# Performance work log

Hardware: AMD Instinct MI355X
Metric: run time of the kernel (lower is better)

Reference implementation:

```python
import jax, jax.numpy as jnp
import numpy as np

B, T, C, L = 512, 512, 96, 64   # batch, time steps, num classes (incl. blank), max label len
BLANK = C - 1                   # keras ctc_batch_cost uses last class as blank
EPS = 1e-7                      # epsilon added before log, as in ctc_batch_cost
NEG = -1e30                     # log-space -inf surrogate


def setup_inputs():
    key = jax.random.key(0)
    k1, k2, k3 = jax.random.split(key, 3)
    # y_pred is a softmax output: positive, rows sum to 1
    u = jax.random.uniform(k1, (B, T, C), dtype=jnp.float32, minval=0.1, maxval=1.0)
    y_pred = u / jnp.sum(u, axis=-1, keepdims=True)
    # labels in [0, BLANK), variable lengths, padded with -1 (as the layer expects)
    labels = jax.random.randint(k2, (B, L), 0, C - 1, dtype=jnp.int32)
    lens = jax.random.randint(k3, (B,), L // 2, L + 1, dtype=jnp.int32)
    y_true = jnp.where(jnp.arange(L)[None, :] < lens[:, None], labels, -1)
    return {"y_true": y_true, "y_pred": y_pred}


def _ctc_loss(y_true, y_pred):
    """Per-example CTC negative log-likelihood (forward DP in log space)."""
    y_true = y_true.astype(jnp.int32)
    lbl_len = jnp.sum((y_true != -1).astype(jnp.int32), axis=-1)          # (B,)
    labels = jnp.where(y_true != -1, y_true, 0)                            # (B,L)

    S = 2 * L + 1
    # extended label: blank, l0, blank, l1, ..., blank
    ext = jnp.full((B, S), BLANK, dtype=jnp.int32).at[:, 1::2].set(labels)  # (B,S)
    ext_m2 = jnp.pad(ext[:, :-2], ((0, 0), (2, 0)), constant_values=BLANK)
    can_skip = (ext != BLANK) & (ext != ext_m2)                             # (B,S)

    lp = jnp.log(y_pred.astype(jnp.float32) + EPS)   # (B,T,C) log-probs
    lp_t = jnp.swapaxes(lp, 0, 1)                    # (T,B,C) for scan over time

    emit0 = jnp.take_along_axis(lp_t[0], ext, axis=1)                       # (B,S)
    alpha0 = (jnp.full((B, S), NEG, dtype=jnp.float32)
              .at[:, 0].set(emit0[:, 0])
              .at[:, 1].set(emit0[:, 1]))

    def step(alpha, lpt):
        a1 = jnp.pad(alpha[:, :-1], ((0, 0), (1, 0)), constant_values=NEG)
        a2 = jnp.pad(alpha[:, :-2], ((0, 0), (2, 0)), constant_values=NEG)
        a2 = jnp.where(can_skip, a2, NEG)
        m = jnp.maximum(alpha, jnp.maximum(a1, a2))
        lse = m + jnp.log(jnp.exp(alpha - m) + jnp.exp(a1 - m) + jnp.exp(a2 - m))
        alpha_new = lse + jnp.take_along_axis(lpt, ext, axis=1)
        return alpha_new, None

    alphaT, _ = jax.lax.scan(step, alpha0, lp_t[1:])

    # total log-prob ends at last blank (s=2*len) or last label (s=2*len-1)
    i_blank = (2 * lbl_len)[:, None]
    i_label = jnp.maximum(2 * lbl_len - 1, 0)[:, None]
    a_b = jnp.take_along_axis(alphaT, i_blank, axis=1)[:, 0]
    a_l = jnp.take_along_axis(alphaT, i_label, axis=1)[:, 0]
    return -jnp.logaddexp(a_b, a_l)                                         # (B,)


def reference(y_true, y_pred):
    # layer adds tf.reduce_mean(ctc_batch_cost(...)) as the model loss
    return jnp.mean(_ctc_loss(y_true, y_pred))
```

## Files before the change

### kernel.cpp

```cpp
#include <hip/hip_runtime.h>


#define B_ 512
#define T_ 512
#define C_ 96
#define L_ 64
#define BLANK_ 95
#define EPSF 1e-7f
#define LN2F 0.69314718055994530942f

#define BARRIER() asm volatile("s_waitcnt lgkmcnt(0)\n\ts_barrier" ::: "memory")

template <int CTRL>
__device__ __forceinline__ float dpp_mov(float x) {
    return __int_as_float(
        __builtin_amdgcn_update_dpp(0, __float_as_int(x), CTRL, 0xF, 0xF, true));
}

__device__ __forceinline__ float wave_max(float m) {
    m = fmaxf(m, dpp_mov<0x111>(m));
    m = fmaxf(m, dpp_mov<0x112>(m));
    m = fmaxf(m, dpp_mov<0x114>(m));
    m = fmaxf(m, dpp_mov<0x118>(m));
    m = fmaxf(m, dpp_mov<0x142>(m));
    m = fmaxf(m, dpp_mov<0x143>(m));
    return __int_as_float(__builtin_amdgcn_readlane(__float_as_int(m), 63));
}

__launch_bounds__(256, 1)
__global__ void ctc_loss_kernel(const int* __restrict__ y_true,
                                const float* __restrict__ y_pred,
                                float* __restrict__ out) {
    const int b = blockIdx.x;
    const int tid = threadIdx.x;
    const int wid = tid >> 6;
    const int lane = tid & 63;

    constexpr int U = 8;
    constexpr int NCH = T_ / U;
    constexpr int CHW = U * C_;

    __shared__ __align__(16) float smem[2 * CHW];

    const float* __restrict__ gb = y_pred + (size_t)b * T_ * C_ + lane * 4;

    int len = 0, lab = 0;
    bool cs = false;
    float a_even = 0.0f, a_odd = 0.0f, a128 = 0.0f;
    int accum = -96;
    float4 rg[3];

    if (wid == 0) {
        const int yv = y_true[b * L_ + lane];
        const unsigned long long act = __ballot(yv != -1);
        len = __popcll(act);
        lab = (yv == -1) ? 0 : yv;
        const int lab_prev = __shfl_up(lab, 1);
        cs = (lane == 0) ? true : (lab != lab_prev);
        a_even = (lane == 0) ? 0x1.0p96f : 0.0f;
    } else {
        const int p = wid - 1;
        const int c0 = (p == 0) ? 0 : p;
#pragma unroll
        for (int j = 0; j < 3; ++j)
            rg[j] = *reinterpret_cast<const float4*>(gb + c0 * CHW + j * 256);
        if (p == 0) {
#pragma unroll
            for (int j = 0; j < 3; ++j)
                *reinterpret_cast<float4*>(&smem[(j * 64 + lane) * 4]) = rg[j];
#pragma unroll
            for (int j = 0; j < 3; ++j)
                rg[j] = *reinterpret_cast<const float4*>(gb + 3 * CHW + j * 256);
        }
    }

    for (int i = 0; i < NCH; ++i) {
        BARRIER();
        if (wid == 0) {
            const float* sl = smem + (i & 1) * CHW;
            float pl[U], pb[U], mpl[U];
#pragma unroll
            for (int k = 0; k < U; ++k) {
                pl[k] = sl[k * C_ + lab] + EPSF;
                pb[k] = sl[k * C_ + BLANK_] + EPSF;
                mpl[k] = cs ? pl[k] : 0.0f;
            }
#pragma unroll
            for (int k = 0; k < U; ++k) {
                const float po = dpp_mov<0x138>(a_odd);
                const float ne = fmaf(po, pb[k], a_even * pb[k]);
                const float no = fmaf(po, mpl[k], (a_odd + a_even) * pl[k]);
                a128 = fmaf(a_odd, pb[k], a128 * pb[k]);
                a_even = ne;
                a_odd = no;
            }
            const float mv = wave_max(fmaxf(fmaxf(a_even, a_odd), a128));
            const int e = ((__float_as_int(mv) >> 23) & 0xFF) - 126;
            const int kk = 96 - e;
            a_even = ldexpf(a_even, kk);
            a_odd = ldexpf(a_odd, kk);
            a128 = ldexpf(a128, kk);
            accum -= kk;
        } else {
            const int p = wid - 1;
            const int cw = i + 1;
            if (cw < NCH && (cw % 3) == p) {
                float* dst = smem + (cw & 1) * CHW;
#pragma unroll
                for (int j = 0; j < 3; ++j)
                    *reinterpret_cast<float4*>(&dst[(j * 64 + lane) * 4]) = rg[j];
                const int nc = cw + 3;
                if (nc < NCH) {
#pragma unroll
                    for (int j = 0; j < 3; ++j)
                        rg[j] = *reinterpret_cast<const float4*>(
                            gb + nc * CHW + j * 256);
                }
            }
        }
    }

    if (wid == 0) {
        const float al = __shfl(a_odd, len - 1);
        const float ab = (len < L_) ? __shfl(a_even, len)
                                    : __shfl(a128, 63);
        if (lane == 0) {
            const float loss = -LN2F * (log2f(ab + al) + (float)accum);
            atomicAdd(out, loss * (1.0f / B_));
        }
    }
}

extern "C" void kernel_launch(void* const* d_in, const int* in_sizes, int n_in,
                              void* d_out, int out_size, void* d_ws, size_t ws_size,
                              hipStream_t stream) {
    const int* y_true = (const int*)d_in[0];
    const float* y_pred = (const float*)d_in[1];
    float* out = (float*)d_out;
    hipMemsetAsync(out, 0, sizeof(float), stream);
    ctc_loss_kernel<<<B_, 256, 0, stream>>>(y_true, y_pred, out);
}
```

Before: 182.8 us.

## Software-pipeline LDS probability reads into registers with a four-slot shared ring

The single consumer wave now loads the next chunk's label and blank probabilities from shared memory into a second register set while it computes the current chunk. This takes LDS read latency off the serial recurrence. To allow it, the shared buffer grows from two to four chunk slots and the producer waves fill two chunks ahead. The block is split into separate consumer and producer loops, each hitting the same number of barriers. This costs more shared memory and more consumer registers, and the last iteration does one extra unused LDS read.

Measured after the change: 176.6 us. 1.04x faster.

```diff
diff --git a/kernel.cpp b/kernel.cpp
--- a/kernel.cpp
+++ b/kernel.cpp
@@ -10,6 +10,7 @@
 #define LN2F 0.69314718055994530942f
 
 #define BARRIER() asm volatile("s_waitcnt lgkmcnt(0)\n\ts_barrier" ::: "memory")
+#define SCHED_FENCE() asm volatile("" ::: "memory")
 
 template <int CTRL>
 __device__ __forceinline__ float dpp_mov(float x) {
@@ -40,93 +41,121 @@
     constexpr int NCH = T_ / U;
     constexpr int CHW = U * C_;
 
-    __shared__ __align__(16) float smem[2 * CHW];
+    __shared__ __align__(16) float smem[4 * CHW];
 
     const float* __restrict__ gb = y_pred + (size_t)b * T_ * C_ + lane * 4;
-
-    int len = 0, lab = 0;
-    bool cs = false;
-    float a_even = 0.0f, a_odd = 0.0f, a128 = 0.0f;
-    int accum = -96;
-    float4 rg[3];
 
     if (wid == 0) {
         const int yv = y_true[b * L_ + lane];
         const unsigned long long act = __ballot(yv != -1);
-        len = __popcll(act);
-        lab = (yv == -1) ? 0 : yv;
+        const int len = __popcll(act);
+        const int lab = (yv == -1) ? 0 : yv;
         const int lab_prev = __shfl_up(lab, 1);
-        cs = (lane == 0) ? true : (lab != lab_prev);
-        a_even = (lane == 0) ? 0x1.0p96f : 0.0f;
-    } else {
-        const int p = wid - 1;
-        const int c0 = (p == 0) ? 0 : p;
+        const bool cs = (lane == 0) ? true : (lab != lab_prev);
+
+        float a_even = (lane == 0) ? 0x1.0p96f : 0.0f;
+        float a_odd = 0.0f, a128 = 0.0f;
+        int accum = -96;
+
+        const float* sl_lab = smem + lab;
+        const float* sl_blk = smem + BLANK_;
+
+        float pl[2][U], pb[2][U];
+
+        BARRIER();
+
 #pragma unroll
-        for (int j = 0; j < 3; ++j)
-            rg[j] = *reinterpret_cast<const float4*>(gb + c0 * CHW + j * 256);
-        if (p == 0) {
+        for (int k = 0; k < U; ++k) {
+            pl[0][k] = sl_lab[k * C_];
+            pb[0][k] = sl_blk[k * C_];
+        }
+        SCHED_FENCE();
+
+        for (int ii = 0; ii < NCH / 4; ++ii) {
 #pragma unroll
-            for (int j = 0; j < 3; ++j)
-                *reinterpret_cast<float4*>(&smem[(j * 64 + lane) * 4]) = rg[j];
+            for (int sub = 0; sub < 4; ++sub) {
+                const int cur = sub & 1, nxt = cur ^ 1;
+                const int nslot = (sub + 1) & 3;
+
 #pragma unroll
-            for (int j = 0; j < 3; ++j)
-                rg[j] = *reinterpret_cast<const float4*>(gb + 3 * CHW + j * 256);
-        }
-    }
+                for (int k = 0; k < U; ++k) {
+                    pl[nxt][k] = sl_lab[nslot * CHW + k * C_];
+                    pb[nxt][k] = sl_blk[nslot * CHW + k * C_];
+                }
+                SCHED_FENCE();
 
-    for (int i = 0; i < NCH; ++i) {
-        BARRIER();
-        if (wid == 0) {
-            const float* sl = smem + (i & 1) * CHW;
-            float pl[U], pb[U], mpl[U];
 #pragma unroll
-            for (int k = 0; k < U; ++k) {
-                pl[k] = sl[k * C_ + lab] + EPSF;
-                pb[k] = sl[k * C_ + BLANK_] + EPSF;
-                mpl[k] = cs ? pl[k] : 0.0f;
-            }
-#pragma unroll
-            for (int k = 0; k < U; ++k) {
-                const float po = dpp_mov<0x138>(a_odd);
-                const float ne = fmaf(po, pb[k], a_even * pb[k]);
-                const float no = fmaf(po, mpl[k], (a_odd + a_even) * pl[k]);
-                a128 = fmaf(a_odd, pb[k], a128 * pb[k]);
-                a_even = ne;
-                a_odd = no;
-            }
-            const float mv = wave_max(fmaxf(fmaxf(a_even, a_odd), a128));
-            const int e = ((__float_as_int(mv) >> 23) & 0xFF) - 126;
-            const int kk = 96 - e;
-            a_even = ldexpf(a_even, kk);
-            a_odd = ldexpf(a_odd, kk);
-            a128 = ldexpf(a128, kk);
-            accum -= kk;
-        } else {
-            const int p = wid - 1;
-            const int cw = i + 1;
-            if (cw < NCH && (cw % 3) == p) {
-                float* dst = smem + (cw & 1) * CHW;
-#pragma unroll
-                for (int j = 0; j < 3; ++j)
-                    *reinterpret_cast<float4*>(&dst[(j * 64 + lane) * 4]) = rg[j];
-                const int nc = cw + 3;
-                if (nc < NCH) {
-#pragma unroll
-                    for (int j = 0; j < 3; ++j)
-                        rg[j] = *reinterpret_cast<const float4*>(
-                            gb + nc * CHW + j * 256);
+                for (int k = 0; k < U; ++k) {
+                    const float plk = pl[cur][k] + EPSF;
+                    const float pbk = pb[cur][k] + EPSF;
+                    const float po = dpp_mov<0x138>(a_odd);
+                    const float ne = fmaf(po, pbk, a_even * pbk);
+                    const float no =
+                        fmaf(po, cs ? plk : 0.0f, (a_odd + a_even) * plk);
+                    a128 = fmaf(a_odd, pbk, a128 * pbk);
+                    a_even = ne;
+                    a_odd = no;
                 }
+
+                const float mv = wave_max(fmaxf(fmaxf(a_even, a_odd), a128));
+                const int e = ((__float_as_int(mv) >> 23) & 0xFF) - 126;
+                const int kk = 96 - e;
+                a_even = ldexpf(a_even, kk);
+                a_odd = ldexpf(a_odd, kk);
+                a128 = ldexpf(a128, kk);
+                accum -= kk;
+
+                BARRIER();
             }
         }
-    }
 
-    if (wid == 0) {
         const float al = __shfl(a_odd, len - 1);
         const float ab = (len < L_) ? __shfl(a_even, len)
                                     : __shfl(a128, 63);
         if (lane == 0) {
             const float loss = -LN2F * (log2f(ab + al) + (float)accum);
             atomicAdd(out, loss * (1.0f / B_));
+        }
+    } else {
+        const int p = wid - 1;
+        const int c0 = (p == 0) ? 0 : p;
+        float4 rg[3];
+#pragma unroll
+        for (int j = 0; j < 3; ++j)
+            rg[j] = *reinterpret_cast<const float4*>(gb + c0 * CHW + j * 256);
+        if (p <= 1) {
+            float* dst = smem + c0 * CHW;
+#pragma unroll
+            for (int j = 0; j < 3; ++j)
+                *reinterpret_cast<float4*>(&dst[(j * 64 + lane) * 4]) = rg[j];
+#pragma unroll
+            for (int j = 0; j < 3; ++j)
+                rg[j] = *reinterpret_cast<const float4*>(gb + (c0 + 3) * CHW +
+                                                         j * 256);
+        }
+        BARRIER();
+
+        for (int ii = 0; ii < NCH / 4; ++ii) {
+#pragma unroll
+            for (int sub = 0; sub < 4; ++sub) {
+                const int i = ii * 4 + sub;
+                const int cw = i + 2;
+                if (cw < NCH && cw % 3 == p) {
+                    float* dst = smem + (cw & 3) * CHW;
+#pragma unroll
+                    for (int j = 0; j < 3; ++j)
+                        *reinterpret_cast<float4*>(&dst[(j * 64 + lane) * 4]) =
+                            rg[j];
+                    const int nc = cw + 3;
+                    if (nc < NCH) {
+#pragma unroll
+                        for (int j = 0; j < 3; ++j)
+                            rg[j] = *reinterpret_cast<const float4*>(
+                                gb + nc * CHW + j * 256);
+                    }
+                }
+                BARRIER();
+            }
         }
     }
 }
```
